# Optimization experiments

Hardware: AMD Instinct MI355X
Metric: run time of the kernel (lower is better)

Reference implementation:

```python
import jax, jax.numpy as jnp
import numpy as np

B, T, HID = 2, 2048, 2048
H, D, QC = 16, 128, 512
RD, THETA = 64, 10000.0
WIN = 512
G, INTER = 4, 2048
EPS = 1e-6


def _rope_cache(t):
    inv = 1.0 / (THETA ** (jnp.arange(0, RD, 2, dtype=jnp.float32) / RD))  # (RD/2,)
    ang = jnp.arange(t, dtype=jnp.float32)[:, None] * inv[None, :]          # (t, RD/2)
    return jnp.cos(ang), jnp.sin(ang)


def _apply_partial_rope(x, cos, sin):
    # x: (..., t, D); rotate first RD channels (rotate-half convention)
    x_rot, x_pass = x[..., :RD], x[..., RD:]
    x1, x2 = x_rot[..., : RD // 2], x_rot[..., RD // 2 :]
    r1 = x1 * cos - x2 * sin
    r2 = x1 * sin + x2 * cos
    return jnp.concatenate([r1, r2, x_pass], axis=-1)


def _rmsnorm(x, w):
    return x * jax.lax.rsqrt(jnp.mean(x * x, axis=-1, keepdims=True) + EPS) * w


def setup_inputs() -> dict:
    key = jax.random.key(0)
    ks = jax.random.split(key, 10)
    s = 0.02
    return {
        "h": jax.random.normal(ks[0], (B, T, HID), jnp.float32),
        "wq_comp": jax.random.normal(ks[1], (HID, QC), jnp.float32) * s,
        "wq_up": jax.random.normal(ks[2], (QC, H * D), jnp.float32) * s,
        "wk": jax.random.normal(ks[3], (HID, D), jnp.float32) * s,
        "wv": jax.random.normal(ks[4], (HID, D), jnp.float32) * s,
        "q_norm_w": jnp.ones((D,), jnp.float32),
        "k_norm_w": jnp.ones((D,), jnp.float32),
        "sink_logit": jnp.zeros((H,), jnp.float32),
        "out_w1": jax.random.normal(ks[5], (G, (H // G) * D, INTER), jnp.float32) * s,
        "out_w2": jax.random.normal(ks[6], (G * INTER, HID), jnp.float32) * s,
    }


def reference(h, wq_comp, wq_up, wk, wv, q_norm_w, k_norm_w, sink_logit, out_w1, out_w2):
    b, t, _ = h.shape
    cos, sin = _rope_cache(t)
    # queries: compress -> up -> (b,H,t,D)
    q = (h @ wq_comp) @ wq_up
    q = q.reshape(b, t, H, D).transpose(0, 2, 1, 3)
    q = _rmsnorm(_apply_partial_rope(q, cos, sin), q_norm_w)
    # single shared K/V head (b,t,D)
    k = _rmsnorm(_apply_partial_rope(h @ wk, cos, sin), k_norm_w)
    v = h @ wv
    i = jnp.arange(t)
    diff = i[:, None] - i[None, :]
    mask = (diff >= 0) & (diff < WIN)  # (t,t)
    # scores (b,H,t,t) + sink column
    scale = 1.0 / jnp.sqrt(jnp.asarray(D, h.dtype))
    scores = jnp.einsum("bhtd,bsd->bhts", q, k) * scale
    scores = jnp.where(mask[None, None], scores, jnp.asarray(-1e30, h.dtype))
    sink = jnp.broadcast_to(sink_logit[None, :, None, None], (b, H, t, 1))
    probs = jax.nn.softmax(jnp.concatenate([scores, sink], axis=-1), axis=-1)
    attn = jnp.einsum("bhts,bsd->bhtd", probs[..., :t], v)  # sink mass dropped
    # grouped output projection
    x = attn.transpose(0, 2, 1, 3).reshape(b, t, G, (H // G) * D)
    x = jnp.einsum("btgi,gio->btgo", x, out_w1).reshape(b, t, G * INTER)
    return x @ out_w2
```

## Files before the change

kernel.cpp:

```cpp
#include <hip/hip_runtime.h>
#include <hip/hip_bf16.h>
#include <stdint.h>

typedef __hip_bfloat16 bf16;
typedef __bf16 bf16x8 __attribute__((ext_vector_type(8)));
typedef float f32x4 __attribute__((ext_vector_type(4)));

#define B_ 2
#define T_ 2048
#define HID_ 2048
#define H_ 16
#define D_ 128
#define WIN_ 512

__device__ __forceinline__ void async_copy16(const void* g, void* l) {
  __builtin_amdgcn_global_load_lds(
      (__attribute__((address_space(1))) void*)(uintptr_t)g,
      (__attribute__((address_space(3))) void*)(uint32_t)(uintptr_t)l,
      16, 0, 0);
}

__global__ __launch_bounds__(256) void cvt4(
    const float* __restrict__ in, bf16* __restrict__ out, int n4)
{
  const int i = blockIdx.x * 256 + threadIdx.x;
  if (i >= n4) return;
  const float4 v = ((const float4*)in)[i];
  bf16* p = out + (size_t)i * 4;
  p[0] = __float2bfloat16(v.x);
  p[1] = __float2bfloat16(v.y);
  p[2] = __float2bfloat16(v.z);
  p[3] = __float2bfloat16(v.w);
}

__global__ __launch_bounds__(256) void cvtT(
    const float* __restrict__ in, bf16* __restrict__ out, int R, int C)
{
  __shared__ bf16 tile[32][33];
  const int bx = blockIdx.x*32, by = blockIdx.y*32;
  const int tx = threadIdx.x & 31, ty = threadIdx.x >> 5;
#pragma unroll
  for (int i = 0; i < 32; i += 8)
    tile[ty+i][tx] = __float2bfloat16(in[(size_t)(by + ty + i)*C + bx + tx]);
  __syncthreads();
#pragma unroll
  for (int i = 0; i < 32; i += 8)
    out[(size_t)(bx + ty + i)*R + by + tx] = tile[tx][ty+i];
}

__global__ __launch_bounds__(256) void transpose_k(
    const bf16* __restrict__ in, bf16* __restrict__ out,
    int R, int C, int ldin, int ldout, long long inBatch, long long outBatch)
{
  __shared__ bf16 tile[32][33];
  in  += (size_t)blockIdx.z * inBatch;
  out += (size_t)blockIdx.z * outBatch;
  const int bx = blockIdx.x*32, by = blockIdx.y*32;
  const int tx = threadIdx.x & 31, ty = threadIdx.x >> 5;
#pragma unroll
  for (int i = 0; i < 32; i += 8)
    tile[ty+i][tx] = in[(size_t)(by + ty + i)*ldin + bx + tx];
  __syncthreads();
#pragma unroll
  for (int i = 0; i < 32; i += 8)
    out[(size_t)(bx + ty + i)*ldout + by + tx] = tile[tx][ty+i];
}

template <bool F32OUT>
__global__ __launch_bounds__(256) void gemm_bt(
    const bf16* __restrict__ Ab, const bf16* __restrict__ Bb, void* __restrict__ Cb,
    int K, int lda, int ldb, int ldc,
    long long sAz, long long sBz, long long sCz)
{
  const bf16* A = Ab + (size_t)blockIdx.z * sAz;
  const bf16* B = Bb + (size_t)blockIdx.z * sBz;
  __shared__ __align__(16) __bf16 sa[128*64];
  __shared__ __align__(16) __bf16 sb[128*64];
  const int bm = blockIdx.x * 128, bn = blockIdx.y * 128;
  const int t = threadIdx.x;
  const int wave = t >> 6, lane = t & 63;
  const int fm = lane & 15, quad = lane >> 4;
  const int wm = (wave & 1) * 64, wn = (wave >> 1) * 64;
  const int arow0 = t >> 3;
  const int acol_sw = (((t & 7) ^ (arow0 & 7)) << 3);
  const int fsw = fm & 7;

  f32x4 acc[4][4];
#pragma unroll
  for (int i = 0; i < 4; ++i)
#pragma unroll
    for (int j = 0; j < 4; ++j) acc[i][j] = {0.f, 0.f, 0.f, 0.f};

  for (int k0 = 0; k0 < K; k0 += 64) {
    __syncthreads();
#pragma unroll
    for (int i = 0; i < 4; ++i)
      async_copy16(&A[(size_t)(bm + arow0 + i*32)*lda + k0 + acol_sw], &sa[(size_t)(i*256 + wave*64)*8]);
#pragma unroll
    for (int i = 0; i < 4; ++i)
      async_copy16(&B[(size_t)(bn + arow0 + i*32)*ldb + k0 + acol_sw], &sb[(size_t)(i*256 + wave*64)*8]);
    __syncthreads();
#pragma unroll
    for (int ks = 0; ks < 64; ks += 32) {
      bf16x8 av[4], bv[4];
#pragma unroll
      for (int mt = 0; mt < 4; ++mt)
        av[mt] = *(const bf16x8*)&sa[(wm + mt*16 + fm)*64 + ((((ks>>3) + quad) ^ fsw) << 3)];
#pragma unroll
      for (int nt = 0; nt < 4; ++nt)
        bv[nt] = *(const bf16x8*)&sb[(wn + nt*16 + fm)*64 + ((((ks>>3) + quad) ^ fsw) << 3)];
#pragma unroll
      for (int mt = 0; mt < 4; ++mt)
#pragma unroll
        for (int nt = 0; nt < 4; ++nt)
          acc[mt][nt] = __builtin_amdgcn_mfma_f32_16x16x32_bf16(av[mt], bv[nt], acc[mt][nt], 0, 0, 0);
    }
  }
  if constexpr (F32OUT) {
    float* C = (float*)Cb + (size_t)blockIdx.z * sCz;
#pragma unroll
    for (int mt = 0; mt < 4; ++mt)
#pragma unroll
      for (int r = 0; r < 4; ++r) {
        const int row = bm + wm + mt*16 + quad*4 + r;
#pragma unroll
        for (int nt = 0; nt < 4; ++nt)
          C[(size_t)row*ldc + bn + wn + nt*16 + fm] = acc[mt][nt][r];
      }
  } else {
    bf16* C = (bf16*)Cb + (size_t)blockIdx.z * sCz;
#pragma unroll
    for (int mt = 0; mt < 4; ++mt)
#pragma unroll
      for (int r = 0; r < 4; ++r) {
        const int row = bm + wm + mt*16 + quad*4 + r;
#pragma unroll
        for (int nt = 0; nt < 4; ++nt)
          C[(size_t)row*ldc + bn + wn + nt*16 + fm] = __float2bfloat16(acc[mt][nt][r]);
      }
  }
}

__global__ __launch_bounds__(256) void rope_rms_kernel(
    const bf16* __restrict__ in, bf16* __restrict__ out, const float* __restrict__ w,
    int in_stride, int out_stride, int t_shift, float oscale)
{
  const int rid = blockIdx.x*4 + (threadIdx.x >> 6);
  const int lane = threadIdx.x & 63;
  const bf16* row = in + (size_t)rid * in_stride;
  float e0 = __bfloat162float(row[lane]);
  float e1 = __bfloat162float(row[lane + 64]);
  float s2 = e0*e0 + e1*e1;
#pragma unroll
  for (int off = 32; off; off >>= 1) s2 += __shfl_xor(s2, off);
  const float rms = rsqrtf(s2 * (1.f/128.f) + 1e-6f) * oscale;
  const int tpos = (rid >> t_shift) & (T_ - 1);
  const int i = lane & 31;
  const float inv = expf(-(float)i * 0.28782313662425574f);
  const float ang = (float)tpos * inv;
  float sn, c;
  sincosf(ang, &sn, &c);
  const float other = __shfl_xor(e0, 32);
  const float r0 = (lane < 32) ? (e0*c - other*sn) : (other*sn + e0*c);
  bf16* orow = out + (size_t)rid * out_stride;
  orow[lane]      = __float2bfloat16(r0 * rms * w[lane]);
  orow[lane + 64] = __float2bfloat16(e1 * rms * w[lane + 64]);
}

__global__ __launch_bounds__(256) void attn_kernel(
    const bf16* __restrict__ q,
    const bf16* __restrict__ k,
    const bf16* __restrict__ vt,
    const float* __restrict__ sink,
    bf16* __restrict__ o)
{
  __shared__ __align__(16) __bf16 sQ[64*128];
  __shared__ __align__(16) __bf16 sK[64*128];
  __shared__ __align__(16) __bf16 sV[128*64];
  __shared__ __align__(16) __bf16 sP[64*72];
  const int qt = blockIdx.x, h = blockIdx.y, b = blockIdx.z;
  const int qb = qt * 64;
  const int t = threadIdx.x, wave = t >> 6, lane = t & 63;
  const int fm = lane & 15, quad = lane >> 4;
  const int fsw = fm & 7;
  const int qw = qb + wave*16;

#pragma unroll
  for (int i = 0; i < 4; ++i) {
    int chunk = i*256 + t;
    int r = chunk >> 4, c8 = (chunk & 15) ^ (r & 7);
    async_copy16(&q[(size_t)((b*T_ + qb + r)*H_ + h)*D_ + c8*8], &sQ[(size_t)(i*256 + wave*64)*8]);
  }
  float l_run[4] = {0.f, 0.f, 0.f, 0.f};
  f32x4 oacc[8];
#pragma unroll
  for (int i = 0; i < 8; ++i) oacc[i] = {0.f, 0.f, 0.f, 0.f};

  int lo = qb - (WIN_ - 1); if (lo < 0) lo = 0;
  for (int kt = lo >> 6; kt <= qt; ++kt) {
    const int kb = kt * 64;
    __syncthreads();
#pragma unroll
    for (int i = 0; i < 4; ++i) {
      int chunk = i*256 + t;
      int r = chunk >> 4, c8 = (chunk & 15) ^ (r & 7);
      async_copy16(&k[(size_t)(b*T_ + kb + r)*D_ + c8*8], &sK[(size_t)(i*256 + wave*64)*8]);
    }
#pragma unroll
    for (int i = 0; i < 4; ++i) {
      int chunk = i*256 + t;
      int d = chunk >> 3, c8 = (chunk & 7) ^ (d & 7);
      async_copy16(&vt[(size_t)(b*D_ + d)*T_ + kb + c8*8], &sV[(size_t)(i*256 + wave*64)*8]);
    }
    __syncthreads();

    f32x4 s[4];
#pragma unroll
    for (int nt = 0; nt < 4; ++nt) s[nt] = {0.f, 0.f, 0.f, 0.f};
#pragma unroll
    for (int ds = 0; ds < 4; ++ds) {
      bf16x8 aq = *(const bf16x8*)&sQ[(wave*16 + fm)*128 + (((ds*4 + quad) ^ fsw) << 3)];
#pragma unroll
      for (int nt = 0; nt < 4; ++nt) {
        bf16x8 bk = *(const bf16x8*)&sK[(nt*16 + fm)*128 + (((ds*4 + quad) ^ fsw) << 3)];
        s[nt] = __builtin_amdgcn_mfma_f32_16x16x32_bf16(aq, bk, s[nt], 0, 0, 0);
      }
    }
    const bool interior = (kb + 63 <= qw) && (kb >= qw - (WIN_ - 16));
    if (!interior) {
      const int qi0 = qb + wave*16 + quad*4;
#pragma unroll
      for (int nt = 0; nt < 4; ++nt) {
        const int ki = kb + nt*16 + fm;
#pragma unroll
        for (int r = 0; r < 4; ++r) {
          const int qi = qi0 + r;
          const bool ok = (ki <= qi) && (qi - ki < WIN_);
          s[nt][r] = ok ? s[nt][r] : -1e30f;
        }
      }
    }
#pragma unroll
    for (int nt = 0; nt < 4; ++nt)
#pragma unroll
      for (int r = 0; r < 4; ++r) {
        const float p = __builtin_exp2f(s[nt][r]);
        l_run[r] += p;
        sP[(wave*16 + quad*4 + r)*72 + nt*16 + fm] = __float2bfloat16(p);
      }
    asm volatile("s_waitcnt lgkmcnt(0)" ::: "memory");
#pragma unroll
    for (int ks = 0; ks < 2; ++ks) {
      bf16x8 ap = *(const bf16x8*)&sP[(wave*16 + fm)*72 + ks*32 + quad*8];
#pragma unroll
      for (int nt = 0; nt < 8; ++nt) {
        bf16x8 bv = *(const bf16x8*)&sV[(nt*16 + fm)*64 + (((ks*4 + quad) ^ fsw) << 3)];
        oacc[nt] = __builtin_amdgcn_mfma_f32_16x16x32_bf16(ap, bv, oacc[nt], 0, 0, 0);
      }
    }
  }
#pragma unroll
  for (int off = 1; off < 16; off <<= 1)
#pragma unroll
    for (int r = 0; r < 4; ++r) l_run[r] += __shfl_xor(l_run[r], off);
  const float sink_p = __builtin_exp2f(sink[h] * 1.4426950408889634f);
#pragma unroll
  for (int r = 0; r < 4; ++r) {
    const int qi = qb + wave*16 + quad*4 + r;
    const float inv_l = 1.f / (l_run[r] + sink_p);
#pragma unroll
    for (int nt = 0; nt < 8; ++nt) {
      const int d = nt*16 + fm;
      o[(size_t)(b*T_ + qi)*(H_*D_) + h*D_ + d] = __float2bfloat16(oacc[nt][r] * inv_l);
    }
  }
}

extern "C" void kernel_launch(void* const* d_in, const int* in_sizes, int n_in,
                              void* d_out, int out_size, void* d_ws, size_t ws_size,
                              hipStream_t stream) {
  (void)in_sizes; (void)n_in; (void)out_size; (void)ws_size;
  const float* h       = (const float*)d_in[0];
  const float* wq_comp = (const float*)d_in[1];
  const float* wq_up   = (const float*)d_in[2];
  const float* wk      = (const float*)d_in[3];
  const float* wv      = (const float*)d_in[4];
  const float* qnw     = (const float*)d_in[5];
  const float* knw     = (const float*)d_in[6];
  const float* sink    = (const float*)d_in[7];
  const float* w1      = (const float*)d_in[8];
  const float* w2      = (const float*)d_in[9];
  float* out = (float*)d_out;
  bf16* ws   = (bf16*)d_ws;

  const size_t M1 = 1048576;
  const size_t o_hb    = 0;
  const size_t o_qr    = 8*M1;
  const size_t o_w2T   = 0;
  const size_t o_qkv   = 16*M1;
  const size_t o_WefT  = 16*M1;
  const size_t o_krt   = 20*M1;
  const size_t o_vt    = 20*M1 + 524288;
  const size_t o_wqkvT = 21*M1;
  const size_t o_wquT  = 22*M1 + 524288;
  const size_t o_w1b   = 23*M1 + 524288;
  const size_t o_x     = 27*M1 + 524288;

  const dim3 tb(256);
  cvt4<<<dim3(8192), tb, 0, stream>>>(h,  ws+o_hb,  2097152);
  cvt4<<<dim3(4096), tb, 0, stream>>>(w1, ws+o_w1b, 1048576);
  cvtT<<<dim3(16, 64), tb, 0, stream>>>(wq_comp, ws+o_wqkvT, 2048, 512);
  cvtT<<<dim3(4, 64),  tb, 0, stream>>>(wk, ws+o_wqkvT + (size_t)512*2048, 2048, 128);
  cvtT<<<dim3(4, 64),  tb, 0, stream>>>(wv, ws+o_wqkvT + (size_t)640*2048, 2048, 128);
  cvtT<<<dim3(64, 16), tb, 0, stream>>>(wq_up, ws+o_wquT, 512, 2048);

  gemm_bt<false><<<dim3(32, 6), tb, 0, stream>>>(ws+o_hb, ws+o_wqkvT, ws+o_qkv,
                                                 2048, 2048, 2048, 768, 0, 0, 0);
  gemm_bt<false><<<dim3(32, 16), tb, 0, stream>>>(ws+o_qkv, ws+o_wquT, ws+o_qr,
                                                  512, 768, 512, 2048, 0, 0, 0);
  rope_rms_kernel<<<dim3(16384), tb, 0, stream>>>(ws+o_qr, ws+o_qr, qnw, 128, 128, 4, 0.12751744f);
  rope_rms_kernel<<<dim3(1024), tb, 0, stream>>>(ws+o_qkv + 512, ws+o_krt, knw, 768, 128, 0, 1.0f);
  transpose_k<<<dim3(4, 64, 2), tb, 0, stream>>>(ws+o_qkv + 640, ws+o_vt, 2048, 128, 768, 2048,
                                                 (long long)2048*768, (long long)128*2048);

  attn_kernel<<<dim3(T_/64, H_, B_), tb, 0, stream>>>(ws+o_qr, ws+o_krt, ws+o_vt, sink, ws+o_x);

  cvtT<<<dim3(64, 256), tb, 0, stream>>>(w2, ws+o_w2T, 8192, 2048);
  gemm_bt<false><<<dim3(16, 4, 4), tb, 0, stream>>>(ws+o_w2T, ws+o_w1b, ws+o_WefT,
                                                    2048, 8192, 2048, 2048,
                                                    2048, (long long)512*2048, 512);
  gemm_bt<true><<<dim3(32, 16), tb, 0, stream>>>(ws+o_x, ws+o_WefT, out,
                                                 2048, 2048, 2048, 2048, 0, 0, 0);
}
```

Before: 370.2 us.

## Add 256x128 8-wave pipelined GEMM and merge small conversion/rope launches

Adds a new bf16 MFMA GEMM with 512 threads, 256x128 block tiles, double-buffered async global-to-LDS loads and interleaved staging, and uses it for the q-up projection, the weight-fold GEMM and the final output GEMM. It also merges the separate fp32-to-bf16 conversion and transpose launches and the two rope/rmsnorm launches into single kernels, which cuts launch count. The larger tiles raise reuse per block but reduce block count and may lower occupancy on some GEMM shapes.

```diff
diff --git a/kernel.cpp b/kernel.cpp
--- a/kernel.cpp
+++ b/kernel.cpp
@@ -20,17 +20,47 @@
       16, 0, 0);
 }
 
-__global__ __launch_bounds__(256) void cvt4(
-    const float* __restrict__ in, bf16* __restrict__ out, int n4)
-{
-  const int i = blockIdx.x * 256 + threadIdx.x;
-  if (i >= n4) return;
+__device__ __forceinline__ void block_sync() {
+  asm volatile("" ::: "memory");
+  __builtin_amdgcn_s_barrier();
+  asm volatile("" ::: "memory");
+}
+
+__global__ __launch_bounds__(256) void cvt4_all(
+    const float* __restrict__ h, const float* __restrict__ w1, bf16* __restrict__ outh, bf16* __restrict__ outw1)
+{
+  int i = blockIdx.x * 256 + threadIdx.x;
+  const int NH = 2097152;
+  const float* in; bf16* out;
+  if (i < NH) { in = h; out = outh; }
+  else { i -= NH; in = w1; out = outw1; }
   const float4 v = ((const float4*)in)[i];
   bf16* p = out + (size_t)i * 4;
   p[0] = __float2bfloat16(v.x);
   p[1] = __float2bfloat16(v.y);
   p[2] = __float2bfloat16(v.z);
   p[3] = __float2bfloat16(v.w);
+}
+
+__global__ __launch_bounds__(256) void cvtT_all(
+    const float* __restrict__ wqc, const float* __restrict__ wk, const float* __restrict__ wv,
+    const float* __restrict__ wqu, bf16* __restrict__ qkvT, bf16* __restrict__ wquT)
+{
+  __shared__ bf16 tile[32][33];
+  const int id = blockIdx.x;
+  const float* in; bf16* out; int R, C, bx, by;
+  if (id < 1024)      { int l = id;        in = wqc; out = qkvT;                      R = 2048; C = 512;  bx = (l & 15) * 32; by = (l >> 4) * 32; }
+  else if (id < 1280) { int l = id - 1024; in = wk;  out = qkvT + (size_t)512 * 2048; R = 2048; C = 128;  bx = (l & 3) * 32;  by = (l >> 2) * 32; }
+  else if (id < 1536) { int l = id - 1280; in = wv;  out = qkvT + (size_t)640 * 2048; R = 2048; C = 128;  bx = (l & 3) * 32;  by = (l >> 2) * 32; }
+  else                { int l = id - 1536; in = wqu; out = wquT;                      R = 512;  C = 2048; bx = (l & 63) * 32; by = (l >> 6) * 32; }
+  const int tx = threadIdx.x & 31, ty = threadIdx.x >> 5;
+#pragma unroll
+  for (int i = 0; i < 32; i += 8)
+    tile[ty+i][tx] = __float2bfloat16(in[(size_t)(by + ty + i)*C + bx + tx]);
+  __syncthreads();
+#pragma unroll
+  for (int i = 0; i < 32; i += 8)
+    out[(size_t)(bx + ty + i)*R + by + tx] = tile[tx][ty+i];
 }
 
 __global__ __launch_bounds__(256) void cvtT(
@@ -141,11 +171,123 @@
   }
 }
 
-__global__ __launch_bounds__(256) void rope_rms_kernel(
-    const bf16* __restrict__ in, bf16* __restrict__ out, const float* __restrict__ w,
-    int in_stride, int out_stride, int t_shift, float oscale)
-{
-  const int rid = blockIdx.x*4 + (threadIdx.x >> 6);
+template <bool F32OUT>
+__global__ __launch_bounds__(512, 2) void gemm_bt8(
+    const bf16* __restrict__ Ab, const bf16* __restrict__ Bb, void* __restrict__ Cb,
+    int K, int lda, int ldb, int ldc,
+    long long sAz, long long sBz, long long sCz)
+{
+  const bf16* A = Ab + (size_t)blockIdx.z * sAz;
+  const bf16* B = Bb + (size_t)blockIdx.z * sBz;
+  __shared__ __align__(16) __bf16 sA[2][256*64];
+  __shared__ __align__(16) __bf16 sB[2][128*64];
+  const int bm = blockIdx.x * 256, bn = blockIdx.y * 128;
+  const int t = threadIdx.x;
+  const int wave = t >> 6, lane = t & 63;
+  const int fm = lane & 15, quad = lane >> 4, fsw = fm & 7;
+  const int wave_m = wave >> 1, wave_n = wave & 1;
+  const int srow = t >> 3;
+  const int cchunk = (t & 7) ^ (srow & 7);
+  const int NT = K >> 6;
+
+  auto stage = [&](int tile, int o) {
+    if (tile >= NT) return;
+    const int par = tile & 1;
+    const int kc = (tile << 6) + (cchunk << 3);
+    if (o < 2) {
+      async_copy16(&B[(size_t)(bn + (o << 6) + srow)*ldb + kc],
+                   &sB[par][(size_t)((o << 6) + wave*8) * 64]);
+    } else {
+      const int h = (o - 2) << 7;
+      async_copy16(&A[(size_t)(bm + h + srow)*lda + kc],
+                   &sA[par][(size_t)(h + wave*8) * 64]);
+      async_copy16(&A[(size_t)(bm + h + 64 + srow)*lda + kc],
+                   &sA[par][(size_t)(h + 64 + wave*8) * 64]);
+    }
+  };
+
+  f32x4 acc[4][4];
+#pragma unroll
+  for (int i = 0; i < 4; ++i)
+#pragma unroll
+    for (int j = 0; j < 4; ++j) acc[i][j] = {0.f, 0.f, 0.f, 0.f};
+
+  stage(0, 0); stage(0, 1); stage(0, 2); stage(0, 3);
+  stage(1, 0); stage(1, 1);
+  asm volatile("s_waitcnt vmcnt(2)" ::: "memory");
+  block_sync();
+
+  for (int d = 0; d < NT; ++d) {
+    const int par = d & 1;
+    bf16x8 bfr[4][2];
+#pragma unroll
+    for (int q = 0; q < 4; ++q) {
+      const int arow = wave_m*64 + q*16 + fm;
+      const bf16x8 a0 = *(const bf16x8*)&sA[par][(size_t)arow*64 + ((quad ^ fsw) << 3)];
+      const bf16x8 a1 = *(const bf16x8*)&sA[par][(size_t)arow*64 + (((4 + quad) ^ fsw) << 3)];
+      if (q == 0) {
+#pragma unroll
+        for (int n = 0; n < 4; ++n) {
+          const int brow = wave_n*64 + n*16 + fm;
+          bfr[n][0] = *(const bf16x8*)&sB[par][(size_t)brow*64 + ((quad ^ fsw) << 3)];
+          bfr[n][1] = *(const bf16x8*)&sB[par][(size_t)brow*64 + (((4 + quad) ^ fsw) << 3)];
+        }
+      }
+      if (q == 0)      stage(d + 1, 2);
+      else if (q == 1) stage(d + 1, 3);
+      else if (q == 2) stage(d + 2, 0);
+      else             stage(d + 2, 1);
+      block_sync();
+      __builtin_amdgcn_s_setprio(1);
+#pragma unroll
+      for (int n = 0; n < 4; ++n)
+        acc[q][n] = __builtin_amdgcn_mfma_f32_16x16x32_bf16(a0, bfr[n][0], acc[q][n], 0, 0, 0);
+#pragma unroll
+      for (int n = 0; n < 4; ++n)
+        acc[q][n] = __builtin_amdgcn_mfma_f32_16x16x32_bf16(a1, bfr[n][1], acc[q][n], 0, 0, 0);
+      __builtin_amdgcn_s_setprio(0);
+      if (q == 3 && d < NT - 1) {
+        if (d == NT - 2) asm volatile("s_waitcnt vmcnt(0)" ::: "memory");
+        else             asm volatile("s_waitcnt vmcnt(2)" ::: "memory");
+      }
+      block_sync();
+    }
+  }
+
+  if constexpr (F32OUT) {
+    float* C = (float*)Cb + (size_t)blockIdx.z * sCz;
+#pragma unroll
+    for (int q = 0; q < 4; ++q)
+#pragma unroll
+      for (int r = 0; r < 4; ++r) {
+        const int row = bm + wave_m*64 + q*16 + quad*4 + r;
+#pragma unroll
+        for (int n = 0; n < 4; ++n)
+          C[(size_t)row*ldc + bn + wave_n*64 + n*16 + fm] = acc[q][n][r];
+      }
+  } else {
+    bf16* C = (bf16*)Cb + (size_t)blockIdx.z * sCz;
+#pragma unroll
+    for (int q = 0; q < 4; ++q)
+#pragma unroll
+      for (int r = 0; r < 4; ++r) {
+        const int row = bm + wave_m*64 + q*16 + quad*4 + r;
+#pragma unroll
+        for (int n = 0; n < 4; ++n)
+          C[(size_t)row*ldc + bn + wave_n*64 + n*16 + fm] = __float2bfloat16(acc[q][n][r]);
+      }
+  }
+}
+
+__global__ __launch_bounds__(256) void rope_rms_all(
+    const bf16* __restrict__ qin, bf16* __restrict__ qout, const float* __restrict__ qw,
+    const bf16* __restrict__ kin, bf16* __restrict__ kout, const float* __restrict__ kw)
+{
+  int blk = blockIdx.x;
+  const bf16* in; bf16* out; const float* w; int in_stride, t_shift; float oscale;
+  if (blk < 16384) { in = qin; out = qout; w = qw; in_stride = 128; t_shift = 4; oscale = 0.12751744f; }
+  else { blk -= 16384; in = kin; out = kout; w = kw; in_stride = 768; t_shift = 0; oscale = 1.0f; }
+  const int rid = blk*4 + (threadIdx.x >> 6);
   const int lane = threadIdx.x & 63;
   const bf16* row = in + (size_t)rid * in_stride;
   float e0 = __bfloat162float(row[lane]);
@@ -162,7 +304,7 @@
   sincosf(ang, &sn, &c);
   const float other = __shfl_xor(e0, 32);
   const float r0 = (lane < 32) ? (e0*c - other*sn) : (other*sn + e0*c);
-  bf16* orow = out + (size_t)rid * out_stride;
+  bf16* orow = out + (size_t)rid * 128;
   orow[lane]      = __float2bfloat16(r0 * rms * w[lane]);
   orow[lane + 64] = __float2bfloat16(e1 * rms * w[lane + 64]);
 }
@@ -307,28 +449,24 @@
   const size_t o_x     = 27*M1 + 524288;
 
   const dim3 tb(256);
-  cvt4<<<dim3(8192), tb, 0, stream>>>(h,  ws+o_hb,  2097152);
-  cvt4<<<dim3(4096), tb, 0, stream>>>(w1, ws+o_w1b, 1048576);
-  cvtT<<<dim3(16, 64), tb, 0, stream>>>(wq_comp, ws+o_wqkvT, 2048, 512);
-  cvtT<<<dim3(4, 64),  tb, 0, stream>>>(wk, ws+o_wqkvT + (size_t)512*2048, 2048, 128);
-  cvtT<<<dim3(4, 64),  tb, 0, stream>>>(wv, ws+o_wqkvT + (size_t)640*2048, 2048, 128);
-  cvtT<<<dim3(64, 16), tb, 0, stream>>>(wq_up, ws+o_wquT, 512, 2048);
+  cvt4_all<<<dim3(12288), tb, 0, stream>>>(h, w1, ws+o_hb, ws+o_w1b);
+  cvtT_all<<<dim3(2560), tb, 0, stream>>>(wq_comp, wk, wv, wq_up, ws+o_wqkvT, ws+o_wquT);
 
   gemm_bt<false><<<dim3(32, 6), tb, 0, stream>>>(ws+o_hb, ws+o_wqkvT, ws+o_qkv,
                                                  2048, 2048, 2048, 768, 0, 0, 0);
-  gemm_bt<false><<<dim3(32, 16), tb, 0, stream>>>(ws+o_qkv, ws+o_wquT, ws+o_qr,
-                                                  512, 768, 512, 2048, 0, 0, 0);
-  rope_rms_kernel<<<dim3(16384), tb, 0, stream>>>(ws+o_qr, ws+o_qr, qnw, 128, 128, 4, 0.12751744f);
-  rope_rms_kernel<<<dim3(1024), tb, 0, stream>>>(ws+o_qkv + 512, ws+o_krt, knw, 768, 128, 0, 1.0f);
+  gemm_bt8<false><<<dim3(16, 16), dim3(512), 0, stream>>>(ws+o_qkv, ws+o_wquT, ws+o_qr,
+                                                          512, 768, 512, 2048, 0, 0, 0);
+  rope_rms_all<<<dim3(17408), tb, 0, stream>>>(ws+o_qr, ws+o_qr, qnw,
+                                               ws+o_qkv + 512, ws+o_krt, knw);
   transpose_k<<<dim3(4, 64, 2), tb, 0, stream>>>(ws+o_qkv + 640, ws+o_vt, 2048, 128, 768, 2048,
                                                  (long long)2048*768, (long long)128*2048);
 
   attn_kernel<<<dim3(T_/64, H_, B_), tb, 0, stream>>>(ws+o_qr, ws+o_krt, ws+o_vt, sink, ws+o_x);
 
   cvtT<<<dim3(64, 256), tb, 0, stream>>>(w2, ws+o_w2T, 8192, 2048);
-  gemm_bt<false><<<dim3(16, 4, 4), tb, 0, stream>>>(ws+o_w2T, ws+o_w1b, ws+o_WefT,
-                                                    2048, 8192, 2048, 2048,
-                                                    2048, (long long)512*2048, 512);
-  gemm_bt<true><<<dim3(32, 16), tb, 0, stream>>>(ws+o_x, ws+o_WefT, out,
-                                                 2048, 2048, 2048, 2048, 0, 0, 0);
-}
+  gemm_bt8<false><<<dim3(8, 4, 4), dim3(512), 0, stream>>>(ws+o_w2T, ws+o_w1b, ws+o_WefT,
+                                                           2048, 8192, 2048, 2048,
+                                                           2048, (long long)512*2048, 512);
+  gemm_bt8<true><<<dim3(16, 16), dim3(512), 0, stream>>>(ws+o_x, ws+o_WefT, out,
+                                                         2048, 2048, 2048, 2048, 0, 0, 0);
+}
```

After: 353.4 us. 4.5% less time.
